# Optimization experiments

Hardware: AMD Instinct MI355X
Metric: run time of the kernel (lower is better)

The kernel has to match this reference:

```python
import jax, jax.numpy as jnp
import numpy as np

EPS = 1e-5

def _bn(h):
    # BatchNorm1d, affine=False, track_running_stats=False -> batch stats, biased var
    m = h.mean(axis=0)
    v = h.var(axis=0)
    return (h - m) * jax.lax.rsqrt(v + EPS)

def _aggregate(x, edge_index):
    # out[i] = sum over edges (i <- j) of x[j]  + x[i] (self loop)
    dst, src = edge_index[0], edge_index[1]
    n = x.shape[0]
    return jax.ops.segment_sum(x[src], dst, num_segments=n) + x

def setup_inputs() -> dict:
    key = jax.random.key(0)
    ks = jax.random.split(key, 12)
    N, F, H, C, E = 100000, 128, 128, 40, 800000
    x = jax.random.normal(ks[0], (N, F), dtype=jnp.float32)
    edge_index = jax.random.randint(ks[1], (2, E), 0, N, dtype=jnp.int64)
    def lin(kw, kb, fan_in, fan_out):
        bound = 1.0 / np.sqrt(fan_in)
        W = jax.random.uniform(kw, (fan_in, fan_out), minval=-bound, maxval=bound, dtype=jnp.float32)
        b = jax.random.uniform(kb, (fan_out,), minval=-bound, maxval=bound, dtype=jnp.float32)
        return W, b
    W0, b0 = lin(ks[2], ks[3], F, H)
    W1, b1 = lin(ks[4], ks[5], H, H)
    W2, b2 = lin(ks[6], ks[7], H, H)
    Wl, bl = lin(ks[8], ks[9], H, C)
    return {"x": x, "edge_index": edge_index, "W0": W0, "b0": b0,
            "W1": W1, "b1": b1, "W2": W2, "b2": b2, "Wl": Wl, "bl": bl}

def reference(x, edge_index, W0, b0, W1, b1, W2, b2, Wl, bl):
    h = x
    for W, b in ((W0, b0), (W1, b1), (W2, b2)):
        h = _aggregate(h, edge_index)          # spmm(A + I, h)
        h = h @ W + b                          # Linear
        h = _bn(h)                             # BatchNorm1d (no affine)
        h = jax.nn.relu(h)
    return h @ Wl + bl
```

## Files before the change

### kernel.cpp

```cpp
#include <hip/hip_runtime.h>
#include <stdint.h>

typedef __attribute__((ext_vector_type(8))) short short8;
typedef __attribute__((ext_vector_type(4))) float floatx4;

static __device__ __forceinline__ float b2f(uint16_t b){
    return __uint_as_float(((uint32_t)b) << 16);
}
static __device__ __forceinline__ uint16_t f2b(float f){
    uint32_t u = __float_as_uint(f);
    return (uint16_t)((u + 0x7fffu + ((u >> 16) & 1u)) >> 16);
}
static __device__ __forceinline__ float blo(uint32_t v){ return __uint_as_float(v << 16); }
static __device__ __forceinline__ float bhi(uint32_t v){ return __uint_as_float(v & 0xffff0000u); }
static __device__ __forceinline__ uint32_t pack2(float a, float b){
    return ((uint32_t)f2b(b) << 16) | (uint32_t)f2b(a);
}

__global__ void k_sentinel(uint32_t* out, int nwords, uint32_t pat){
    int i = blockIdx.x * blockDim.x + threadIdx.x;
    if (i < nwords) out[i] = pat;
}

__global__ void k_zf(int* deg, int N, const uint32_t* xw, const int* ei, int* flags,
                     float* stats, int ZB){
    if ((int)blockIdx.x == ZB){
        if (threadIdx.x != 0) return;
        int odd_nz = 0;
        for (int k = 0; k < 128; k++){
            if (ei[2 * k + 1] != 0) odd_nz = 1;
        }
        flags[0] = odd_nz ? 0 : 1;
        int big = 0;
        for (int k = 0; k < 128; k++){
            float lo = __uint_as_float(xw[k] << 16);
            if (!(fabsf(lo) <= 1024.0f)) big = 1;
        }
        flags[1] = big ? 0 : 1;
        return;
    }
    if ((int)blockIdx.x == ZB + 1){
        int t = threadIdx.x;
        #pragma unroll
        for (int j = 0; j < 3; j++) stats[j * 256 + t] = 0.f;
        return;
    }
    int i = blockIdx.x * blockDim.x + threadIdx.x;
    if (i < N) deg[i] = 0;
}

__global__ void k_deg(const int* ei, int E, int* deg, uint16_t* rank, const int* flags){
    int e = blockIdx.x * blockDim.x + threadIdx.x;
    if (e < E){
        int d = flags[0] ? ei[2 * e] : ei[e];
        int r = atomicAdd(&deg[d], 1);
        rank[e] = (uint16_t)r;
    }
}

__global__ void k_scan1(const int* deg, int N, int* bsum){
    __shared__ int s[256];
    int t = threadIdx.x;
    int i = blockIdx.x * 256 + t;
    s[t] = (i < N) ? deg[i] : 0;
    __syncthreads();
    for (int off = 128; off > 0; off >>= 1){
        if (t < off) s[t] += s[t + off];
        __syncthreads();
    }
    if (t == 0) bsum[blockIdx.x] = s[0];
}

__global__ void k_scan2(int* bsum, int nb, int* rp, int N){
    __shared__ int s[512];
    int t = threadIdx.x;
    int v = (t < nb) ? bsum[t] : 0;
    s[t] = v;
    __syncthreads();
    for (int off = 1; off < 512; off <<= 1){
        int u = (t >= off) ? s[t - off] : 0;
        __syncthreads();
        s[t] += u;
        __syncthreads();
    }
    if (t < nb) bsum[t] = s[t] - v;
    if (t == 511) rp[N] = s[511];
}

__global__ void k_scan3(const int* deg, int N, const int* bpre, int* rp){
    __shared__ int s[256];
    int t = threadIdx.x;
    int i = blockIdx.x * 256 + t;
    int v = (i < N) ? deg[i] : 0;
    s[t] = v;
    __syncthreads();
    for (int off = 1; off < 256; off <<= 1){
        int u = (t >= off) ? s[t - off] : 0;
        __syncthreads();
        s[t] += u;
        __syncthreads();
    }
    if (i < N) rp[i] = bpre[blockIdx.x] + s[t] - v;
}

__global__ __launch_bounds__(256) void k_fill(const int* __restrict__ ei, int E,
                                              const int* __restrict__ rp,
                                              const uint16_t* __restrict__ rank,
                                              int* __restrict__ col,
                                              const int* __restrict__ flags, int N){
    int xcd = blockIdx.x & 7;
    int sub = blockIdx.x >> 3;
    int nsub = gridDim.x >> 3;
    int r0 = (int)(((long long)N * xcd) >> 3);
    int r1 = (int)(((long long)N * (xcd + 1)) >> 3);
    int e0 = (int)(((long long)E * sub) / nsub);
    int e1 = (int)(((long long)E * (sub + 1)) / nsub);
    int is64 = flags[0];
    for (int e = e0 + threadIdx.x; e < e1; e += 256){
        int d = is64 ? ei[2 * e] : ei[e];
        if (d >= r0 && d < r1){
            int sv = is64 ? ei[2 * (E + e)] : ei[E + e];
            int p = rp[d] + (int)rank[e];
            col[p] = sv;
        }
    }
}

__global__ void k_prep(const void* W0, const void* W1, const void* W2, const void* Wl,
                       uint16_t* Wf0, uint16_t* Wf1, uint16_t* Wf2, uint16_t* Wfl,
                       const void* b0, const void* b1, const void* b2, const void* bl,
                       float* bc, const void* x, uint16_t* hx, int NF,
                       const int* flags){
    int blk = blockIdx.x;
    int t = threadIdx.x;
    if (blk >= 218){
        if (flags[1]) return;
        int nb = gridDim.x - 218;
        int n8 = NF >> 3;
        const float4* xv = (const float4*)x;
        uint4* hv = (uint4*)hx;
        for (int i = (blk - 218) * 256 + t; i < n8; i += nb * 256){
            float4 u0 = xv[i * 2];
            float4 u1 = xv[i * 2 + 1];
            uint4 o;
            o.x = pack2(u0.x, u0.y); o.y = pack2(u0.z, u0.w);
            o.z = pack2(u1.x, u1.y); o.w = pack2(u1.z, u1.w);
            hv[i] = o;
        }
        return;
    }
    if (blk >= 216){
        int i = (blk - 216) * 256 + t;
        if (i >= 424) return;
        const void* src; int li;
        if (i < 128)      { src = b0; li = i; }
        else if (i < 256) { src = b1; li = i - 128; }
        else if (i < 384) { src = b2; li = i - 256; }
        else              { src = bl; li = i - 384; }
        bc[i] = flags[1] ? b2f(((const uint16_t*)src)[li]) : ((const float*)src)[li];
        return;
    }
    const void* W; uint16_t* Wf; int C, ntiles, lb;
    if (blk < 64)        { W = W0; Wf = Wf0; C = 128; ntiles = 8; lb = blk; }
    else if (blk < 128)  { W = W1; Wf = Wf1; C = 128; ntiles = 8; lb = blk - 64; }
    else if (blk < 192)  { W = W2; Wf = Wf2; C = 128; ntiles = 8; lb = blk - 128; }
    else                 { W = Wl; Wf = Wfl; C = 40;  ntiles = 3; lb = blk - 192; }
    int idx = lb * 256 + t;
    int total = 4 * ntiles * 512;
    if (idx >= total) return;
    int j = idx & 7;
    int lane = (idx >> 3) & 63;
    int nt = (idx >> 9) % ntiles;
    int kt = idx / (512 * ntiles);
    int k = kt * 32 + (lane >> 4) * 8 + j;
    int n = nt * 16 + (lane & 15);
    uint16_t v = 0;
    if (n < C){
        v = flags[1] ? ((const uint16_t*)W)[k * C + n]
                     : f2b(((const float*)W)[k * C + n]);
    }
    Wf[idx] = v;
}

__global__ __launch_bounds__(256) void k_agg(const uint16_t* __restrict__ Yin,
                                             const uint16_t* __restrict__ xraw,
                                             const int* __restrict__ rp,
                                             const int* __restrict__ col,
                                             uint16_t* __restrict__ out, int N,
                                             const float* __restrict__ st,
                                             int apply_bn, float ninv,
                                             const int* __restrict__ flags){
    int t = threadIdx.x;
    int l16 = t & 15;
    int i = blockIdx.x * 16 + (t >> 4);
    if (i >= N) return;
    float tt[8], iv[8];
    const uint16_t* src = Yin;
    if (apply_bn){
        int f0 = l16 * 8;
        #pragma unroll
        for (int j = 0; j < 8; j++){
            float sv = st[f0 + j];
            float qv = st[128 + f0 + j];
            float m = sv * ninv;
            float var = qv * ninv - m * m;
            float ivj = rsqrtf(var + 1e-5f);
            iv[j] = ivj;
            tt[j] = -m * ivj;
        }
    } else if (flags[1]){
        src = xraw;
    }
    const uint4* base = (const uint4*)src;
    int s0 = rp[i], e0 = rp[i + 1];
    float a[8];
    {
        uint4 w = base[(size_t)i * 16 + l16];
        a[0] = blo(w.x); a[1] = bhi(w.x); a[2] = blo(w.y); a[3] = bhi(w.y);
        a[4] = blo(w.z); a[5] = bhi(w.z); a[6] = blo(w.w); a[7] = bhi(w.w);
        if (apply_bn){
            #pragma unroll
            for (int jj = 0; jj < 8; jj++) a[jj] = fmaxf(fmaf(a[jj], iv[jj], tt[jj]), 0.f);
        }
    }
    int k = s0;
    for (; k + 3 < e0; k += 4){
        int j0 = col[k], j1 = col[k + 1], j2 = col[k + 2], j3 = col[k + 3];
        uint4 ww[4];
        ww[0] = base[(size_t)j0 * 16 + l16];
        ww[1] = base[(size_t)j1 * 16 + l16];
        ww[2] = base[(size_t)j2 * 16 + l16];
        ww[3] = base[(size_t)j3 * 16 + l16];
        #pragma unroll
        for (int u = 0; u < 4; u++){
            float v[8] = {blo(ww[u].x), bhi(ww[u].x), blo(ww[u].y), bhi(ww[u].y),
                          blo(ww[u].z), bhi(ww[u].z), blo(ww[u].w), bhi(ww[u].w)};
            if (apply_bn){
                #pragma unroll
                for (int jj = 0; jj < 8; jj++) v[jj] = fmaxf(fmaf(v[jj], iv[jj], tt[jj]), 0.f);
            }
            #pragma unroll
            for (int jj = 0; jj < 8; jj++) a[jj] += v[jj];
        }
    }
    for (; k < e0; k++){
        int j = col[k];
        uint4 w = base[(size_t)j * 16 + l16];
        float v[8] = {blo(w.x), bhi(w.x), blo(w.y), bhi(w.y),
                      blo(w.z), bhi(w.z), blo(w.w), bhi(w.w)};
        if (apply_bn){
            #pragma unroll
            for (int jj = 0; jj < 8; jj++) v[jj] = fmaxf(fmaf(v[jj], iv[jj], tt[jj]), 0.f);
        }
        #pragma unroll
        for (int jj = 0; jj < 8; jj++) a[jj] += v[jj];
    }
    uint4 o;
    o.x = pack2(a[0], a[1]); o.y = pack2(a[2], a[3]);
    o.z = pack2(a[4], a[5]); o.w = pack2(a[6], a[7]);
    ((uint4*)out)[(size_t)i * 16 + l16] = o;
}

__global__ __launch_bounds__(256) void k_gemm(uint16_t* __restrict__ A,
                                              const uint16_t* __restrict__ Wf,
                                              const float* __restrict__ bias,
                                              float* __restrict__ part, int N){
    __shared__ __align__(16) uint16_t wlds[16384];
    __shared__ float sh_sum[128], sh_ssq[128];
    int t = threadIdx.x;
    if (t < 128){ sh_sum[t] = 0.f; sh_ssq[t] = 0.f; }
    {
        const uint4* s = (const uint4*)Wf;
        uint4* d = (uint4*)wlds;
        for (int i = t; i < 2048; i += 256) d[i] = s[i];
    }
    __syncthreads();
    int lane = t & 63, wave = t >> 6;
    int m = lane & 15, q = lane >> 4;
    int rb[2];
    rb[0] = blockIdx.x * 128 + wave * 16;
    rb[1] = rb[0] + 64;
    short8 afrag[2][4];
    #pragma unroll
    for (int mt = 0; mt < 2; mt++){
        int arow = rb[mt] + m;
        if (arow >= N) arow = N - 1;
        const short8* ap = (const short8*)(A + (size_t)arow * 128);
        #pragma unroll
        for (int kt = 0; kt < 4; kt++) afrag[mt][kt] = ap[kt * 4 + q];
    }
    floatx4 acc[2][8];
    #pragma unroll
    for (int mt = 0; mt < 2; mt++)
        #pragma unroll
        for (int nt = 0; nt < 8; nt++) acc[mt][nt] = (floatx4){0.f, 0.f, 0.f, 0.f};
    const short8* wl = (const short8*)wlds;
    #pragma unroll
    for (int kt = 0; kt < 4; kt++){
        #pragma unroll
        for (int nt = 0; nt < 8; nt++){
            short8 bfrag = wl[(kt * 8 + nt) * 64 + lane];
            #pragma unroll
            for (int mt = 0; mt < 2; mt++){
                acc[mt][nt] = __builtin_amdgcn_mfma_f32_16x16x32_bf16(afrag[mt][kt], bfrag, acc[mt][nt], 0, 0, 0);
            }
        }
    }
    #pragma unroll
    for (int mt = 0; mt < 2; mt++){
        #pragma unroll
        for (int nt = 0; nt < 8; nt++){
            int ccol = nt * 16 + m;
            float bv = bias[ccol];
            float s = 0.f, ss = 0.f;
            #pragma unroll
            for (int r = 0; r < 4; r++){
                int grow = rb[mt] + q * 4 + r;
                if (grow < N){
                    float y = acc[mt][nt][r] + bv;
                    A[(size_t)grow * 128 + ccol] = f2b(y);
                    s += y;
                    ss += y * y;
                }
            }
            s += __shfl_xor(s, 16); s += __shfl_xor(s, 32);
            ss += __shfl_xor(ss, 16); ss += __shfl_xor(ss, 32);
            if (q == 0){
                atomicAdd(&sh_sum[ccol], s);
                atomicAdd(&sh_ssq[ccol], ss);
            }
        }
    }
    __syncthreads();
    if (t < 128){
        part[(size_t)blockIdx.x * 256 + t] = sh_sum[t];
        part[(size_t)blockIdx.x * 256 + 128 + t] = sh_ssq[t];
    }
}

__global__ __launch_bounds__(256) void k_red(const float* __restrict__ part, int nb,
                                             float* __restrict__ st){
    int t = threadIdx.x;
    int r0 = blockIdx.x * 32;
    int r1 = r0 + 32; if (r1 > nb) r1 = nb;
    float s0 = 0.f, s1 = 0.f, s2 = 0.f, s3 = 0.f;
    int b = r0;
    for (; b + 3 < r1; b += 4){
        s0 += part[(size_t)b * 256 + t];
        s1 += part[(size_t)(b + 1) * 256 + t];
        s2 += part[(size_t)(b + 2) * 256 + t];
        s3 += part[(size_t)(b + 3) * 256 + t];
    }
    for (; b < r1; b++) s0 += part[(size_t)b * 256 + t];
    atomicAdd(&st[t], (s0 + s1) + (s2 + s3));
}

__global__ __launch_bounds__(256) void k_out(const uint16_t* __restrict__ A,
                                             const uint16_t* __restrict__ Wf,
                                             const float* __restrict__ bias,
                                             const float* __restrict__ st, float ninv,
                                             void* __restrict__ out, int N,
                                             const int* __restrict__ flags){
    __shared__ __align__(16) uint16_t wlds[6144];
    __shared__ float s_m[128], s_iv[128];
    int t = threadIdx.x;
    {
        const uint4* s = (const uint4*)Wf;
        uint4* d = (uint4*)wlds;
        for (int i = t; i < 768; i += 256) d[i] = s[i];
    }
    if (t < 128){
        float m = st[t] * ninv;
        float var = st[128 + t] * ninv - m * m;
        s_m[t] = m;
        s_iv[t] = rsqrtf(var + 1e-5f);
    }
    __syncthreads();
    int lane = t & 63, wave = t >> 6;
    int m = lane & 15, q = lane >> 4;
    int row_base = blockIdx.x * 64 + wave * 16;
    int arow = row_base + m;
    if (arow >= N) arow = N - 1;
    short8 afrag[4];
    const uint4* ap = (const uint4*)(A + (size_t)arow * 128);
    #pragma unroll
    for (int kt = 0; kt < 4; kt++){
        uint4 u = ap[kt * 4 + q];
        float v[8] = {blo(u.x), bhi(u.x), blo(u.y), bhi(u.y),
                      blo(u.z), bhi(u.z), blo(u.w), bhi(u.w)};
        int c0 = kt * 32 + q * 8;
        #pragma unroll
        for (int j = 0; j < 8; j++) v[j] = fmaxf((v[j] - s_m[c0 + j]) * s_iv[c0 + j], 0.f);
        uint4 o;
        o.x = pack2(v[0], v[1]); o.y = pack2(v[2], v[3]);
        o.z = pack2(v[4], v[5]); o.w = pack2(v[6], v[7]);
        afrag[kt] = *(short8*)&o;
    }
    floatx4 acc[3];
    #pragma unroll
    for (int nt = 0; nt < 3; nt++) acc[nt] = (floatx4){0.f, 0.f, 0.f, 0.f};
    const short8* wl = (const short8*)wlds;
    #pragma unroll
    for (int kt = 0; kt < 4; kt++){
        #pragma unroll
        for (int nt = 0; nt < 3; nt++){
            acc[nt] = __builtin_amdgcn_mfma_f32_16x16x32_bf16(afrag[kt], wl[(kt * 3 + nt) * 64 + lane], acc[nt], 0, 0, 0);
        }
    }
    int isbf = flags[1];
    #pragma unroll
    for (int nt = 0; nt < 3; nt++){
        int ccol = nt * 16 + m;
        if (ccol < 40){
            float bv = bias[ccol];
            #pragma unroll
            for (int r = 0; r < 4; r++){
                int grow = row_base + q * 4 + r;
                if (grow < N){
                    float y = acc[nt][r] + bv;
                    if (isbf) ((uint16_t*)out)[(size_t)grow * 40 + ccol] = f2b(y);
                    else      ((float*)out)[(size_t)grow * 40 + ccol] = y;
                }
            }
        }
    }
}

extern "C" void kernel_launch(void* const* d_in, const int* in_sizes, int n_in,
                              void* d_out, int out_size, void* d_ws, size_t ws_size,
                              hipStream_t stream){
    (void)n_in;
    const void* x  = d_in[0];
    const int* ei  = (const int*)d_in[1];
    const void* W0 = d_in[2];
    const void* b0 = d_in[3];
    const void* W1 = d_in[4];
    const void* b1 = d_in[5];
    const void* W2 = d_in[6];
    const void* b2 = d_in[7];
    const void* Wl = d_in[8];
    const void* bl = d_in[9];

    const int N = in_sizes[0] / 128;
    const int E = in_sizes[1] / 2;
    const int NF = N * 128;
    const int NB = (N + 255) / 256;
    const int agg_blocks   = (N + 15) / 16;
    const int gemm_blocks2 = (N + 127) / 128;
    const int gemm_blocks  = (N + 63) / 64;
    const int red_blocks   = (gemm_blocks2 + 31) / 32;

    char* ws = (char*)d_ws;
    size_t off = 0;
    uint16_t* hx = (uint16_t*)(ws + off); off += ((size_t)NF * 2 + 255) & ~(size_t)255;
    uint16_t* ag = (uint16_t*)(ws + off); off += ((size_t)NF * 2 + 255) & ~(size_t)255;
    int* col     = (int*)(ws + off);      off += ((size_t)E * 4 + 255) & ~(size_t)255;
    int* rp      = (int*)(ws + off);      off += ((size_t)(N + 1) * 4 + 255) & ~(size_t)255;
    uint16_t* rank = (uint16_t*)(ws + off); off += ((size_t)E * 2 + 255) & ~(size_t)255;
    int* deg     = (int*)(ws + off);      off += ((size_t)N * 4 + 255) & ~(size_t)255;
    int* bsum    = (int*)(ws + off);      off += 512 * 4;
    int* flags   = (int*)(ws + off);      off += 256;
    uint16_t* Wf0 = (uint16_t*)(ws + off); off += 16384 * 2;
    uint16_t* Wf1 = (uint16_t*)(ws + off); off += 16384 * 2;
    uint16_t* Wf2 = (uint16_t*)(ws + off); off += 16384 * 2;
    uint16_t* Wfl = (uint16_t*)(ws + off); off += 6144 * 2;
    float* bc    = (float*)(ws + off);    off += 424 * 4 + 160;
    float* stats = (float*)(ws + off);    off += 768 * 4;
    float* part  = (float*)(ws + off);    off += (size_t)gemm_blocks2 * 256 * 4;
    const size_t required = off;

    if (ws_size < required){
        int nwords = out_size / 2;
        k_sentinel<<<(nwords + 255) / 256, 256, 0, stream>>>((uint32_t*)d_out, nwords, 0x40004000u);
        return;
    }

    k_zf<<<NB + 2, 256, 0, stream>>>(deg, N, (const uint32_t*)x, ei, flags, stats, NB);
    k_deg<<<(E + 255) / 256, 256, 0, stream>>>(ei, E, deg, rank, flags);
    k_scan1<<<NB, 256, 0, stream>>>(deg, N, bsum);
    k_scan2<<<1, 512, 0, stream>>>(bsum, NB, rp, N);
    k_scan3<<<NB, 256, 0, stream>>>(deg, N, bsum, rp);
    k_fill<<<1024, 256, 0, stream>>>(ei, E, rp, rank, col, flags, N);

    k_prep<<<2266, 256, 0, stream>>>(W0, W1, W2, Wl, Wf0, Wf1, Wf2, Wfl,
                                     b0, b1, b2, bl, bc, x, hx, NF, flags);

    const float ninv = 1.0f / (float)N;
    const uint16_t* xr = (const uint16_t*)x;

    k_agg<<<agg_blocks, 256, 0, stream>>>(hx, xr, rp, col, ag, N, stats, 0, ninv, flags);
    k_gemm<<<gemm_blocks2, 256, 0, stream>>>(ag, Wf0, bc, part, N);
    k_red<<<red_blocks, 256, 0, stream>>>(part, gemm_blocks2, stats);
    k_agg<<<agg_blocks, 256, 0, stream>>>(ag, xr, rp, col, hx, N, stats, 1, ninv, flags);
    k_gemm<<<gemm_blocks2, 256, 0, stream>>>(hx, Wf1, bc + 128, part, N);
    k_red<<<red_blocks, 256, 0, stream>>>(part, gemm_blocks2, stats + 256);
    k_agg<<<agg_blocks, 256, 0, stream>>>(hx, xr, rp, col, ag, N, stats + 256, 1, ninv, flags);
    k_gemm<<<gemm_blocks2, 256, 0, stream>>>(ag, Wf2, bc + 256, part, N);
    k_red<<<red_blocks, 256, 0, stream>>>(part, gemm_blocks2, stats + 512);
    k_out<<<gemm_blocks, 256, 0, stream>>>(ag, Wfl, bc + 384, stats + 512, ninv, d_out, N, flags);
}
```

Baseline: 384.9 us.

## Store features in 16-column chunked layout and aggregate per chunk

Feature matrices change from row-major [N,128] bf16 to eight column chunks of [N,16]. Each aggregation block now handles one chunk for 128 rows, so the gathered working set per pass (100k rows × 32 bytes, about 3.2 MB) is meant to fit in cache and cut DRAM traffic for the random neighbour gathers. GEMM and output kernels are updated to read and write the chunked layout, and col indices use nontemporal loads. The cost is that each row's rp and col entries are now read eight times, and every gather is only 32 bytes long.

Measured after the change: 503.5 us. 1.31x slower.

```diff
diff --git a/kernel.cpp b/kernel.cpp
--- a/kernel.cpp
+++ b/kernel.cpp
@@ -129,23 +129,36 @@
 __global__ void k_prep(const void* W0, const void* W1, const void* W2, const void* Wl,
                        uint16_t* Wf0, uint16_t* Wf1, uint16_t* Wf2, uint16_t* Wfl,
                        const void* b0, const void* b1, const void* b2, const void* bl,
-                       float* bc, const void* x, uint16_t* hx, int NF,
+                       float* bc, const void* x, uint16_t* hx, int N,
                        const int* flags){
     int blk = blockIdx.x;
     int t = threadIdx.x;
     if (blk >= 218){
-        if (flags[1]) return;
         int nb = gridDim.x - 218;
-        int n8 = NF >> 3;
-        const float4* xv = (const float4*)x;
-        uint4* hv = (uint4*)hx;
-        for (int i = (blk - 218) * 256 + t; i < n8; i += nb * 256){
-            float4 u0 = xv[i * 2];
-            float4 u1 = xv[i * 2 + 1];
-            uint4 o;
-            o.x = pack2(u0.x, u0.y); o.y = pack2(u0.z, u0.w);
-            o.z = pack2(u1.x, u1.y); o.w = pack2(u1.z, u1.w);
-            hv[i] = o;
+        int bi = blk - 218;
+        int half2 = N * 2;
+        int isbf = flags[1];
+        for (int c = 0; c < 8; c++){
+            uint4* dst = (uint4*)(hx + (size_t)c * N * 16);
+            if (isbf){
+                const uint16_t* xb = (const uint16_t*)x;
+                for (int idx = bi * 256 + t; idx < half2; idx += nb * 256){
+                    int row = idx >> 1, h = idx & 1;
+                    dst[idx] = *(const uint4*)(xb + (size_t)row * 128 + c * 16 + h * 8);
+                }
+            } else {
+                const float* xf = (const float*)x;
+                for (int idx = bi * 256 + t; idx < half2; idx += nb * 256){
+                    int row = idx >> 1, h = idx & 1;
+                    const float4* s = (const float4*)(xf + (size_t)row * 128 + c * 16 + h * 8);
+                    float4 u0 = s[0];
+                    float4 u1 = s[1];
+                    uint4 o;
+                    o.x = pack2(u0.x, u0.y); o.y = pack2(u0.z, u0.w);
+                    o.z = pack2(u1.x, u1.y); o.w = pack2(u1.z, u1.w);
+                    dst[idx] = o;
+                }
+            }
         }
         return;
     }
@@ -182,22 +195,22 @@
     Wf[idx] = v;
 }
 
-__global__ __launch_bounds__(256) void k_agg(const uint16_t* __restrict__ Yin,
-                                             const uint16_t* __restrict__ xraw,
-                                             const int* __restrict__ rp,
-                                             const int* __restrict__ col,
-                                             uint16_t* __restrict__ out, int N,
-                                             const float* __restrict__ st,
-                                             int apply_bn, float ninv,
-                                             const int* __restrict__ flags){
-    int t = threadIdx.x;
-    int l16 = t & 15;
-    int i = blockIdx.x * 16 + (t >> 4);
+__global__ __launch_bounds__(256) void k_aggc(const uint16_t* __restrict__ Yin,
+                                              const int* __restrict__ rp,
+                                              const int* __restrict__ col,
+                                              uint16_t* __restrict__ out,
+                                              int N, int RT,
+                                              const float* __restrict__ st,
+                                              int apply_bn, float ninv){
+    int t = threadIdx.x;
+    int c = blockIdx.x / RT;
+    int tile = blockIdx.x - c * RT;
+    int r = t >> 1, h = t & 1;
+    int i = tile * 128 + r;
     if (i >= N) return;
     float tt[8], iv[8];
-    const uint16_t* src = Yin;
     if (apply_bn){
-        int f0 = l16 * 8;
+        int f0 = c * 16 + h * 8;
         #pragma unroll
         for (int j = 0; j < 8; j++){
             float sv = st[f0 + j];
@@ -208,14 +221,12 @@
             iv[j] = ivj;
             tt[j] = -m * ivj;
         }
-    } else if (flags[1]){
-        src = xraw;
-    }
-    const uint4* base = (const uint4*)src;
+    }
+    const uint4* base = (const uint4*)(Yin + (size_t)c * N * 16);
     int s0 = rp[i], e0 = rp[i + 1];
     float a[8];
     {
-        uint4 w = base[(size_t)i * 16 + l16];
+        uint4 w = base[(size_t)i * 2 + h];
         a[0] = blo(w.x); a[1] = bhi(w.x); a[2] = blo(w.y); a[3] = bhi(w.y);
         a[4] = blo(w.z); a[5] = bhi(w.z); a[6] = blo(w.w); a[7] = bhi(w.w);
         if (apply_bn){
@@ -225,12 +236,15 @@
     }
     int k = s0;
     for (; k + 3 < e0; k += 4){
-        int j0 = col[k], j1 = col[k + 1], j2 = col[k + 2], j3 = col[k + 3];
+        int j0 = __builtin_nontemporal_load(col + k);
+        int j1 = __builtin_nontemporal_load(col + k + 1);
+        int j2 = __builtin_nontemporal_load(col + k + 2);
+        int j3 = __builtin_nontemporal_load(col + k + 3);
         uint4 ww[4];
-        ww[0] = base[(size_t)j0 * 16 + l16];
-        ww[1] = base[(size_t)j1 * 16 + l16];
-        ww[2] = base[(size_t)j2 * 16 + l16];
-        ww[3] = base[(size_t)j3 * 16 + l16];
+        ww[0] = base[(size_t)j0 * 2 + h];
+        ww[1] = base[(size_t)j1 * 2 + h];
+        ww[2] = base[(size_t)j2 * 2 + h];
+        ww[3] = base[(size_t)j3 * 2 + h];
         #pragma unroll
         for (int u = 0; u < 4; u++){
             float v[8] = {blo(ww[u].x), bhi(ww[u].x), blo(ww[u].y), bhi(ww[u].y),
@@ -244,8 +258,8 @@
         }
     }
     for (; k < e0; k++){
-        int j = col[k];
-        uint4 w = base[(size_t)j * 16 + l16];
+        int j = __builtin_nontemporal_load(col + k);
+        uint4 w = base[(size_t)j * 2 + h];
         float v[8] = {blo(w.x), bhi(w.x), blo(w.y), bhi(w.y),
                       blo(w.z), bhi(w.z), blo(w.w), bhi(w.w)};
         if (apply_bn){
@@ -258,7 +272,7 @@
     uint4 o;
     o.x = pack2(a[0], a[1]); o.y = pack2(a[2], a[3]);
     o.z = pack2(a[4], a[5]); o.w = pack2(a[6], a[7]);
-    ((uint4*)out)[(size_t)i * 16 + l16] = o;
+    ((uint4*)(out + (size_t)c * N * 16))[(size_t)i * 2 + h] = o;
 }
 
 __global__ __launch_bounds__(256) void k_gemm(uint16_t* __restrict__ A,
@@ -285,9 +299,12 @@
     for (int mt = 0; mt < 2; mt++){
         int arow = rb[mt] + m;
         if (arow >= N) arow = N - 1;
-        const short8* ap = (const short8*)(A + (size_t)arow * 128);
-        #pragma unroll
-        for (int kt = 0; kt < 4; kt++) afrag[mt][kt] = ap[kt * 4 + q];
+        #pragma unroll
+        for (int kt = 0; kt < 4; kt++){
+            int cc = 2 * kt + (q >> 1);
+            afrag[mt][kt] = *(const short8*)(A + (size_t)cc * N * 16
+                                               + (size_t)arow * 16 + (q & 1) * 8);
+        }
     }
     floatx4 acc[2][8];
     #pragma unroll
@@ -318,7 +335,7 @@
                 int grow = rb[mt] + q * 4 + r;
                 if (grow < N){
                     float y = acc[mt][nt][r] + bv;
-                    A[(size_t)grow * 128 + ccol] = f2b(y);
+                    A[(size_t)nt * N * 16 + (size_t)grow * 16 + m] = f2b(y);
                     s += y;
                     ss += y * y;
                 }
@@ -382,10 +399,10 @@
     int arow = row_base + m;
     if (arow >= N) arow = N - 1;
     short8 afrag[4];
-    const uint4* ap = (const uint4*)(A + (size_t)arow * 128);
     #pragma unroll
     for (int kt = 0; kt < 4; kt++){
-        uint4 u = ap[kt * 4 + q];
+        uint4 u = *(const uint4*)(A + (size_t)(2 * kt + (q >> 1)) * N * 16
+                                    + (size_t)arow * 16 + (q & 1) * 8);
         float v[8] = {blo(u.x), bhi(u.x), blo(u.y), bhi(u.y),
                       blo(u.z), bhi(u.z), blo(u.w), bhi(u.w)};
         int c0 = kt * 32 + q * 8;
@@ -445,8 +462,9 @@
     const int E = in_sizes[1] / 2;
     const int NF = N * 128;
     const int NB = (N + 255) / 256;
-    const int agg_blocks   = (N + 15) / 16;
-    const int gemm_blocks2 = (N + 127) / 128;
+    const int RT = (N + 127) / 128;
+    const int aggc_grid    = 8 * RT;
+    const int gemm_blocks2 = RT;
     const int gemm_blocks  = (N + 63) / 64;
     const int red_blocks   = (gemm_blocks2 + 31) / 32;
 
@@ -483,18 +501,17 @@
     k_fill<<<1024, 256, 0, stream>>>(ei, E, rp, rank, col, flags, N);
 
     k_prep<<<2266, 256, 0, stream>>>(W0, W1, W2, Wl, Wf0, Wf1, Wf2, Wfl,
-                                     b0, b1, b2, bl, bc, x, hx, NF, flags);
+                                     b0, b1, b2, bl, bc, x, hx, N, flags);
 
     const float ninv = 1.0f / (float)N;
-    const uint16_t* xr = (const uint16_t*)x;
-
-    k_agg<<<agg_blocks, 256, 0, stream>>>(hx, xr, rp, col, ag, N, stats, 0, ninv, flags);
+
+    k_aggc<<<aggc_grid, 256, 0, stream>>>(hx, rp, col, ag, N, RT, stats, 0, ninv);
     k_gemm<<<gemm_blocks2, 256, 0, stream>>>(ag, Wf0, bc, part, N);
     k_red<<<red_blocks, 256, 0, stream>>>(part, gemm_blocks2, stats);
-    k_agg<<<agg_blocks, 256, 0, stream>>>(ag, xr, rp, col, hx, N, stats, 1, ninv, flags);
+    k_aggc<<<aggc_grid, 256, 0, stream>>>(ag, rp, col, hx, N, RT, stats, 1, ninv);
     k_gemm<<<gemm_blocks2, 256, 0, stream>>>(hx, Wf1, bc + 128, part, N);
     k_red<<<red_blocks, 256, 0, stream>>>(part, gemm_blocks2, stats + 256);
-    k_agg<<<agg_blocks, 256, 0, stream>>>(hx, xr, rp, col, ag, N, stats + 256, 1, ninv, flags);
+    k_aggc<<<aggc_grid, 256, 0, stream>>>(hx, rp, col, ag, N, RT, stats + 256, 1, ninv);
     k_gemm<<<gemm_blocks2, 256, 0, stream>>>(ag, Wf2, bc + 256, part, N);
     k_red<<<red_blocks, 256, 0, stream>>>(part, gemm_blocks2, stats + 512);
     k_out<<<gemm_blocks, 256, 0, stream>>>(ag, Wfl, bc + 384, stats + 512, ninv, d_out, N, flags);
```
